# Optimization experiments

Measured on AMD Instinct MI355X. Metric: run time of the kernel, lower is better.

The kernel has to match this reference:

```python
import jax, jax.numpy as jnp
import numpy as np

H = 8
HD = 128
D = 1024
SCALE = 0.12
EOT = 50256
LN_EPS = 1e-6
THETA = 1024.0


def _layernorm(x, w):
    mu = jnp.mean(x, axis=-1, keepdims=True)
    var = jnp.mean(jnp.square(x - mu), axis=-1, keepdims=True)
    return (x - mu) * jax.lax.rsqrt(var + LN_EPS) * w


def _rmsnorm(x):
    eps = jnp.finfo(x.dtype).eps
    return x * jax.lax.rsqrt(jnp.mean(jnp.square(x), axis=-1, keepdims=True) + eps)


def _rope_tables(seq_len, head_dim):
    # half-truncated RoPE: only first half of the rotation pairs get nonzero freqs
    n = head_dim // 4
    freqs = (1.0 / THETA) ** jnp.linspace(0.0, 1.0, n)
    ang = jnp.concatenate([freqs, jnp.zeros((n,), freqs.dtype)])  # [head_dim//2]
    th = jnp.arange(seq_len, dtype=jnp.float32)[:, None] * ang[None, :]
    return jnp.cos(th), jnp.sin(th)  # each [S, head_dim//2]


def _apply_rope(x, cos, sin):
    # x: [B, S, H, hd]
    x1, x2 = jnp.split(x, 2, axis=-1)
    c = cos[None, :, None, :]
    s = sin[None, :, None, :]
    return jnp.concatenate([x1 * c + x2 * s, -x1 * s + x2 * c], axis=-1)


def setup_inputs() -> dict:
    key = jax.random.key(0)
    ks = jax.random.split(key, 10)
    B, S = 2, 2048
    return {
        "x": jax.random.normal(ks[0], (B, S, D), jnp.float32),
        "value_embed": jax.random.normal(ks[1], (S, D), jnp.float32),
        "x0": jax.random.normal(ks[2], (B, S, D), jnp.float32),
        "lambdas": jax.random.uniform(ks[3], (2,), jnp.float32),
        "sa_lambdas": jax.random.uniform(ks[4], (2,), jnp.float32),
        "ln1_w": jnp.ones((D,), jnp.float32),
        "ln2_w": jnp.ones((D,), jnp.float32),
        "w_qkv": jax.random.normal(ks[5], (D, 3 * D), jnp.float32) * 0.02,
        "w_o": jax.random.normal(ks[6], (D, D), jnp.float32) * 0.02,
        "w_fc": jax.random.normal(ks[7], (D, 4 * D), jnp.float32) * 0.02,
        "w_proj": jax.random.normal(ks[8], (4 * D, D), jnp.float32) * 0.02,
        "input_ids": jax.random.randint(ks[9], (S,), 0, 50257, jnp.int64),
    }


def reference(x, value_embed, x0, lambdas, sa_lambdas, ln1_w, ln2_w,
              w_qkv, w_o, w_fc, w_proj, input_ids):
    B, S, Dm = x.shape
    # U-Net residual mixing
    x = lambdas[0] * x + lambdas[1] * x0

    # attention branch
    xn = _layernorm(x, ln1_w)
    qkv = xn @ w_qkv                                # [B,S,3D]
    q, k, v = jnp.split(qkv, 3, axis=-1)
    q = q.reshape(B, S, H, HD)
    k = k.reshape(B, S, H, HD)
    v = v.reshape(B, S, H, HD)

    cos, sin = _rope_tables(S, HD)
    q = _apply_rope(q, cos, sin)
    k = _apply_rope(k, cos, sin)

    # value-embedding mixing
    ve = value_embed.reshape(S, H, HD)[None]        # [1,S,H,hd]
    v = sa_lambdas[0] * v + sa_lambdas[1] * ve

    # QK norm (unit-weight RMSNorm)
    q = _rmsnorm(q)
    k = _rmsnorm(k)

    # document-aware causal mask
    docs = jnp.cumsum(input_ids == EOT)
    idx = jnp.arange(S)
    mask = (idx[:, None] >= idx[None, :]) & (docs[:, None] == docs[None, :])

    scores = jnp.einsum("bqhd,bkhd->bhqk", q, k) * SCALE
    scores = jnp.where(mask[None, None], scores, -jnp.inf)
    attn = jax.nn.softmax(scores, axis=-1)
    out = jnp.einsum("bhqk,bkhd->bqhd", attn, v).reshape(B, S, Dm)
    x = x + out @ w_o

    # MLP with relu^2
    xn = _layernorm(x, ln2_w)
    h = jnp.square(jax.nn.relu(xn @ w_fc))
    x = x + h @ w_proj
    return x
```

## Files before the change

### kernel.cpp

```cpp
#include <hip/hip_runtime.h>

#define EOT_ID 50256

typedef __attribute__((ext_vector_type(8))) short bf16x8;
typedef __attribute__((ext_vector_type(4))) float f32x4;
typedef __attribute__((ext_vector_type(16))) float f32x16;

#define GLOAD_LDS(g, l)                                                        \
  __builtin_amdgcn_global_load_lds(                                            \
      (const __attribute__((address_space(1))) unsigned int*)(g),              \
      (__attribute__((address_space(3))) unsigned int*)(l), 16, 0, 0)

__device__ __forceinline__ unsigned short f2bf(float f) {
  union { float f; unsigned int u; } v; v.f = f;
  unsigned int r = v.u + 0x7FFFu + ((v.u >> 16) & 1u);
  return (unsigned short)(r >> 16);
}
__device__ __forceinline__ float bf2f(unsigned short b) {
  union { unsigned int u; float f; } v; v.u = ((unsigned int)b) << 16;
  return v.f;
}
__device__ __forceinline__ unsigned int cvtpk(float lo, float hi) {
  unsigned int r;
  asm("v_cvt_pk_bf16_f32 %0, %1, %2" : "=v"(r) : "v"(lo), "v"(hi));
  return r;
}
__device__ __forceinline__ void plswap(unsigned int& a, unsigned int& b) {
  asm volatile("v_permlane32_swap_b32 %0, %1" : "+v"(a), "+v"(b));
}
union U8 { unsigned int u[4]; bf16x8 v; };

__global__ void rope_tab_kernel(float* __restrict__ ct, float* __restrict__ st) {
  const int idx = blockIdx.x * 256 + threadIdx.x;
  const int s = idx >> 5, i = idx & 31;
  const float ang = (float)s * exp2f(-10.0f * (float)i / 31.0f);
  float sv, cv;
  sincosf(ang, &sv, &cv);
  ct[idx] = cv;
  st[idx] = sv;
}

__global__ __launch_bounds__(1024)
void docs_kernel(const int* __restrict__ ids, int* __restrict__ qstart) {
  __shared__ int a[2048], b2[2048];
  const int t = threadIdx.x;
  for (int i = t; i < 2048; i += 1024)
    a[i] = (ids[i] == EOT_ID) ? i : 0;
  __syncthreads();
  int* cur = a; int* nxt = b2;
  for (int off = 1; off < 2048; off <<= 1) {
    for (int i = t; i < 2048; i += 1024) {
      int v = cur[i];
      if (i >= off) { int u = cur[i - off]; v = (u > v) ? u : v; }
      nxt[i] = v;
    }
    __syncthreads();
    int* tmp = cur; cur = nxt; nxt = tmp;
  }
  for (int i = t; i < 2048; i += 1024) qstart[i] = cur[i];
}

__global__ __launch_bounds__(256)
void wtrans_kernel(const float* __restrict__ in, unsigned short* __restrict__ out,
                   int K, int N) {
  __shared__ float tile[32][33];
  const int nb = N >> 5;
  const int k0 = (blockIdx.x / nb) << 5, n0 = (blockIdx.x % nb) << 5;
  const int tx = threadIdx.x & 31, ty = threadIdx.x >> 5;
#pragma unroll
  for (int p = 0; p < 4; p++)
    tile[ty + p * 8][tx] = in[(size_t)(k0 + ty + p * 8) * N + n0 + tx];
  __syncthreads();
#pragma unroll
  for (int p = 0; p < 4; p++)
    out[(size_t)(n0 + ty + p * 8) * K + k0 + tx] = f2bf(tile[tx][ty + p * 8]);
}

template<bool MIX>
__global__ __launch_bounds__(256)
void ln_kernel(const float* __restrict__ x, const float* __restrict__ x0,
               const float* __restrict__ lam, const float* __restrict__ w,
               float* __restrict__ xm, unsigned short* __restrict__ xn) {
  __shared__ float red[8];
  const int row = blockIdx.x, t = threadIdx.x;
  const size_t base = (size_t)row << 10;
  float4 v = *(const float4*)(x + base + t * 4);
  if (MIX) {
    const float l0 = lam[0], l1 = lam[1];
    const float4 v0 = *(const float4*)(x0 + base + t * 4);
    v.x = l0 * v.x + l1 * v0.x;
    v.y = l0 * v.y + l1 * v0.y;
    v.z = l0 * v.z + l1 * v0.z;
    v.w = l0 * v.w + l1 * v0.w;
    *(float4*)(xm + base + t * 4) = v;
  }
  float s = v.x + v.y + v.z + v.w;
  float q = v.x * v.x + v.y * v.y + v.z * v.z + v.w * v.w;
#pragma unroll
  for (int off = 1; off < 64; off <<= 1) {
    s += __shfl_xor(s, off);
    q += __shfl_xor(q, off);
  }
  const int wid = t >> 6;
  if ((t & 63) == 0) { red[wid] = s; red[4 + wid] = q; }
  __syncthreads();
  s = red[0] + red[1] + red[2] + red[3];
  q = red[4] + red[5] + red[6] + red[7];
  const float mu = s * (1.0f / 1024.0f);
  const float var = q * (1.0f / 1024.0f) - mu * mu;
  const float rstd = rsqrtf(var + 1e-6f);
  const float4 wv = *(const float4*)(w + t * 4);
  ushort4 u;
  u.x = f2bf((v.x - mu) * rstd * wv.x);
  u.y = f2bf((v.y - mu) * rstd * wv.y);
  u.z = f2bf((v.z - mu) * rstd * wv.z);
  u.w = f2bf((v.w - mu) * rstd * wv.w);
  *(ushort4*)(xn + base + t * 4) = u;
}

template<int EPI, int BM, int BK>
__global__ __launch_bounds__(256, 4)
void gemm_bt(const unsigned short* __restrict__ A,
             const unsigned short* __restrict__ Bt,
             void* __restrict__ Cout,
             const float* __restrict__ res,
             int M, int N, int K) {
  __shared__ unsigned short As[2][BM * BK];
  __shared__ unsigned short Bs[2][128 * BK];
  const int t = threadIdx.x;
  const int wid = t >> 6;
  const int lane = t & 63;
  const int ln = lane & 15, kg = lane >> 4;
  const int nbm = M / BM;
  const int xcd = (int)blockIdx.x & 7, rr = (int)blockIdx.x >> 3;
  const int slab = nbm >> 3;
  const int bm = xcd * slab + (rr % slab);
  const int bn = rr / slab;
  const int m0 = bm * BM, n0 = bn << 7;
  const int wrow = (BM == 128) ? ((wid >> 1) * 64) : 0;
  const int wcol = (BM == 128) ? ((wid & 1) * 64) : (wid * 32);
  constexpr int NJ = (BM == 128) ? 4 : 2;
  constexpr int LA = BM * BK / 2048;
  constexpr int LB = 128 * BK / 2048;
  constexpr int KC = BK / 32;

  f32x4 acc[4][NJ] = {};

  const unsigned short* Abase = A + (size_t)m0 * K;
  const unsigned short* Bbase = Bt + (size_t)n0 * K;

  auto swz = [&](int row, int chunk) -> int {
    if constexpr (BK == 32) return chunk ^ ((row >> 1) & 3);
    else                    return chunk ^ (row & 7);
  };

  auto STAGE = [&](int bb, int kt) {
#pragma unroll
    for (int p = 0; p < LA; p++) {
      const int e = t * 8 + p * 2048;
      const int r = e / BK;
      const int cs = swz(r, (e >> 3) & (BK / 8 - 1));
      GLOAD_LDS(Abase + (size_t)r * K + kt + cs * 8, &As[bb][p * 2048 + wid * 512]);
    }
#pragma unroll
    for (int p = 0; p < LB; p++) {
      const int e = t * 8 + p * 2048;
      const int r = e / BK;
      const int cs = swz(r, (e >> 3) & (BK / 8 - 1));
      GLOAD_LDS(Bbase + (size_t)r * K + kt + cs * 8, &Bs[bb][p * 2048 + wid * 512]);
    }
  };

  STAGE(0, 0);
  int cur = 0;
  const int nk = K / BK;
  for (int ki = 0; ki < nk; ki++) {
    if (ki + 1 < nk) {
      STAGE(cur ^ 1, (ki + 1) * BK);
      if constexpr (LA + LB == 4)
        asm volatile("s_waitcnt vmcnt(4)" ::: "memory");
      else
        asm volatile("s_waitcnt vmcnt(6)" ::: "memory");
    } else {
      asm volatile("s_waitcnt vmcnt(0)" ::: "memory");
    }
    __builtin_amdgcn_s_barrier();

#pragma unroll
    for (int c = 0; c < KC; c++) {
      bf16x8 af[4], bfr[NJ];
#pragma unroll
      for (int i = 0; i < 4; i++) {
        const int ra = wrow + i * 16 + ln;
        af[i] = *(const bf16x8*)(&As[cur][ra * BK + swz(ra, c * 4 + kg) * 8]);
      }
#pragma unroll
      for (int j = 0; j < NJ; j++) {
        const int rb = wcol + j * 16 + ln;
        bfr[j] = *(const bf16x8*)(&Bs[cur][rb * BK + swz(rb, c * 4 + kg) * 8]);
      }
#pragma unroll
      for (int i = 0; i < 4; i++)
#pragma unroll
        for (int j = 0; j < NJ; j++)
          acc[i][j] = __builtin_amdgcn_mfma_f32_16x16x32_bf16(af[i], bfr[j], acc[i][j], 0, 0, 0);
    }

    __builtin_amdgcn_s_barrier();
    cur ^= 1;
  }

#pragma unroll
  for (int i = 0; i < 4; i++) {
#pragma unroll
    for (int j = 0; j < NJ; j++) {
#pragma unroll
      for (int r = 0; r < 4; r++) {
        const int row = m0 + wrow + i * 16 + kg * 4 + r;
        const int col = n0 + wcol + j * 16 + ln;
        const size_t idx = (size_t)row * N + col;
        float v = acc[i][j][r];
        if (EPI == 0) {
          ((float*)Cout)[idx] = v;
        } else if (EPI == 1) {
          ((float*)Cout)[idx] = v + res[idx];
        } else if (EPI == 2) {
          v = fmaxf(v, 0.0f);
          ((unsigned short*)Cout)[idx] = f2bf(v * v);
        } else {
          ((unsigned short*)Cout)[idx] = f2bf(v);
        }
      }
    }
  }
}

__global__ __launch_bounds__(256)
void rope_rms_kernel(const unsigned short* __restrict__ qkv,
                     const float* __restrict__ ct, const float* __restrict__ st,
                     const float* __restrict__ ve, const float* __restrict__ salam,
                     unsigned short* __restrict__ Qh, unsigned short* __restrict__ Kh,
                     unsigned short* __restrict__ Vt) {
  const int t = threadIdx.x;
  const int wid = t >> 6, i = t & 63;
  const int g = blockIdx.x * 4 + wid;
  const int b = g >> 14;
  const int s = (g >> 3) & 2047;
  const int h = g & 7;
  const unsigned short* base = qkv + (size_t)(b * 2048 + s) * 3072 + h * 128;
  float c = 1.0f, sn = 0.0f;
  if (i < 32) { c = ct[s * 32 + i]; sn = st[s * 32 + i]; }
  const float q1 = bf2f(base[i]), q2 = bf2f(base[64 + i]);
  const float k1 = bf2f(base[1024 + i]), k2 = bf2f(base[1024 + 64 + i]);
  const float q1r = q1 * c + q2 * sn, q2r = q2 * c - q1 * sn;
  const float k1r = k1 * c + k2 * sn, k2r = k2 * c - k1 * sn;
  float sq = q1r * q1r + q2r * q2r;
  float sk = k1r * k1r + k2r * k2r;
#pragma unroll
  for (int off = 1; off < 64; off <<= 1) {
    sq += __shfl_xor(sq, off);
    sk += __shfl_xor(sk, off);
  }
  const float eps = 1.1920929e-7f;
  const float rq = rsqrtf(sq * (1.0f / 128.0f) + eps);
  const float rk = rsqrtf(sk * (1.0f / 128.0f) + eps);
  unsigned short* qp = Qh + (((size_t)(b * 2048 + s) * 8 + h) << 7);
  unsigned short* kp = Kh + (((size_t)(b * 2048 + s) * 8 + h) << 7);
  qp[i] = f2bf(q1r * rq); qp[64 + i] = f2bf(q2r * rq);
  kp[i] = f2bf(k1r * rk); kp[64 + i] = f2bf(k2r * rk);
  const float l0 = salam[0], l1 = salam[1];
  const float* vep = ve + (size_t)s * 1024 + h * 128;
  const float v1 = l0 * bf2f(base[2048 + i]) + l1 * vep[i];
  const float v2 = l0 * bf2f(base[2048 + 64 + i]) + l1 * vep[64 + i];
  unsigned short* vp = Vt + (((size_t)(b * 8 + h) * 128) << 11) + s;
  vp[(size_t)i << 11] = f2bf(v1);
  vp[(size_t)(64 + i) << 11] = f2bf(v2);
}

__global__ __launch_bounds__(256, 2)
void attn_kernel(const unsigned short* __restrict__ Qh,
                 const unsigned short* __restrict__ Kh,
                 const unsigned short* __restrict__ Vt,
                 const int* __restrict__ qstart,
                 unsigned short* __restrict__ Out) {
  __shared__ char smem[65536];

  const int blk = blockIdx.x;
  const int p_ = blk >> 4;
  const int qt = (p_ < 16) ? (31 - p_) : (p_ - 16);
  const int bh = blk & 15;
  const int b = bh >> 3, h = bh & 7;
  const int q0 = qt << 6;
  const int t = threadIdx.x;
  const int wid = t >> 6, lane = t & 63;
  const int qw = wid & 1, kw = wid >> 1;
  const int ln5 = lane & 31, hi = lane >> 5;
  const int qrow = q0 + qw * 32;
  const int tp = qw * 64 + lane;

  bf16x8 qf[8];
  {
    const unsigned short* qp =
        Qh + (((size_t)(b * 2048 + qrow + ln5) * 8 + h) << 7) + hi * 8;
#pragma unroll
    for (int c = 0; c < 8; c++) qf[c] = *(const bf16x8*)(qp + c * 16);
  }
  const int qid = qrow + ln5;
  const int qs = qstart[qid];
  int qsmax = qs;
#pragma unroll
  for (int off = 1; off < 32; off <<= 1)
    qsmax = max(qsmax, __shfl_xor(qsmax, off));

  float m = -64.0f, l = 0.0f;
  f32x16 o[4] = {};

  const int kt0 = qstart[q0] & ~31;
  const int T = (q0 + 64 - kt0) >> 5;
  const float SC = 0.12f * 1.4426950408889634f;

  unsigned short* Kb = (unsigned short*)(smem + kw * 16384);
  unsigned short* Vb = (unsigned short*)(smem + 32768 + kw * 16384);

  auto STAGE = [&](int bb, int kt) {
#pragma unroll
    for (int r = 0; r < 4; r++) {
      const int e = tp * 16 + r * 2048;
      const int row = e >> 8;
      const int ch = (e >> 4) & 15;
      const int sch = ch ^ ((row ^ (row >> 3)) & 7);
      GLOAD_LDS(Kh + (((size_t)(b * 2048 + kt + row) * 8 + h) << 7) + sch * 8,
                (char*)Kb + bb * 8192 + r * 2048 + qw * 1024 + (lane << 4));
    }
#pragma unroll
    for (int r = 0; r < 4; r++) {
      const int e = tp * 16 + r * 2048;
      const int row = e >> 6;
      const int ch = (e >> 4) & 3;
      const int sch = ch ^ ((row >> 1) & 3);
      GLOAD_LDS(Vt + (((size_t)((b * 8 + h) * 128 + row)) << 11) + kt + sch * 8,
                (char*)Vb + bb * 8192 + r * 2048 + qw * 1024 + (lane << 4));
    }
  };

  STAGE(0, kt0 + kw * 32);
  int cur = 0;
  const int nLoop = (T + 1) >> 1;

  for (int i = 0; i < nLoop; i++) {
    const int tid = 2 * i + kw;
    const bool hasnext = (tid + 2) < T;
    if (hasnext) {
      STAGE(cur ^ 1, kt0 + (tid + 2) * 32);
      asm volatile("s_waitcnt vmcnt(8)" ::: "memory");
    } else {
      asm volatile("s_waitcnt vmcnt(0)" ::: "memory");
    }
    __builtin_amdgcn_s_barrier();

    if (tid < T) {
      const int kt = kt0 + tid * 32;
      const unsigned short* ksb = (const unsigned short*)((char*)Kb + cur * 8192);
      const unsigned short* vsb = (const unsigned short*)((char*)Vb + cur * 8192);

      f32x16 sacc = {};
      {
        const int key = ln5;
        const int kx = (key ^ (key >> 3)) & 7;
        const unsigned short* krow = &ksb[key * 128];
#pragma unroll
        for (int c = 0; c < 8; c++) {
          bf16x8 kf = *(const bf16x8*)(krow + (((2 * c + hi) ^ kx) << 3));
          sacc = __builtin_amdgcn_mfma_f32_32x32x16_bf16(kf, qf[c], sacc, 0, 0, 0);
        }
      }

      const bool full = (kt + 32 <= qrow) && (kt >= qsmax);

      float p[16];
      float mx = -1e30f;
      if (full) {
#pragma unroll
        for (int i2 = 0; i2 < 16; i2++) {
          const float ts = sacc[i2] * SC;
          p[i2] = ts;
          mx = fmaxf(mx, ts);
        }
      } else {
#pragma unroll
        for (int i2 = 0; i2 < 16; i2++) {
          const int key = kt + (i2 & 3) + 8 * (i2 >> 2) + 4 * hi;
          const bool valid = (key <= qid) && (key >= qs);
          const float ts = valid ? sacc[i2] * SC : -1e30f;
          p[i2] = ts;
          mx = fmaxf(mx, ts);
        }
      }
      mx = fmaxf(mx, __shfl_xor(mx, 32));

      const bool dresc = __any(mx - m > 8.0f);
      if (dresc) {
        const float mn = fmaxf(m, mx);
        const float fac = exp2f(m - mn);
        m = mn;
        l *= fac;
#pragma unroll
        for (int r = 0; r < 16; r++) {
          const float fr = __shfl(fac, (r & 3) + 8 * (r >> 2) + 4 * hi);
          o[0][r] *= fr; o[1][r] *= fr; o[2][r] *= fr; o[3][r] *= fr;
        }
      }

      float sum = 0.0f;
#pragma unroll
      for (int i2 = 0; i2 < 16; i2++) {
        const float pv = exp2f(p[i2] - m);
        p[i2] = pv;
        sum += pv;
      }
      sum += __shfl_xor(sum, 32);
      l += sum;

      bf16x8 pa[2];
#pragma unroll
      for (int bb2 = 0; bb2 < 2; bb2++) {
        unsigned int a0 = cvtpk(p[bb2 * 8 + 0], p[bb2 * 8 + 1]);
        unsigned int b0 = cvtpk(p[bb2 * 8 + 4], p[bb2 * 8 + 5]);
        unsigned int a1 = cvtpk(p[bb2 * 8 + 2], p[bb2 * 8 + 3]);
        unsigned int b1 = cvtpk(p[bb2 * 8 + 6], p[bb2 * 8 + 7]);
        plswap(a0, b0);
        plswap(a1, b1);
        U8 u; u.u[0] = a0; u.u[1] = a1; u.u[2] = b0; u.u[3] = b1;
        pa[bb2] = u.v;
      }

#pragma unroll
      for (int dt = 0; dt < 4; dt++) {
        const int d = dt * 32 + ln5;
        const int dx = (d >> 1) & 3;
        const unsigned short* vrow = &vsb[d * 32];
#pragma unroll
        for (int ks = 0; ks < 2; ks++) {
          bf16x8 vf = *(const bf16x8*)(vrow + (((2 * ks + hi) ^ dx) << 3));
          o[dt] = __builtin_amdgcn_mfma_f32_32x32x16_bf16(pa[ks], vf, o[dt], 0, 0, 0);
        }
      }
    }

    __builtin_amdgcn_s_barrier();
    cur ^= 1;
  }

  __syncthreads();
  float* oex = (float*)smem;
  float* mlx = (float*)(smem + 32768);
  if (kw == 1) {
    if (lane < 32) {
      mlx[(qw * 32 + lane) * 2 + 0] = m;
      mlx[(qw * 32 + lane) * 2 + 1] = l;
    }
    float* dst = oex + (qw * 64 + lane) * 64;
#pragma unroll
    for (int dt = 0; dt < 4; dt++)
#pragma unroll
      for (int r = 0; r < 16; r++) dst[dt * 16 + r] = o[dt][r];
  }
  __syncthreads();
  if (kw == 0) {
    const float m1 = mlx[(qw * 32 + ln5) * 2 + 0];
    const float l1 = mlx[(qw * 32 + ln5) * 2 + 1];
    const float ms = fmaxf(m, m1);
    const float a0 = exp2f(m - ms), a1 = exp2f(m1 - ms);
    const float inv = 1.0f / (l * a0 + l1 * a1);
    const float* src = oex + (qw * 64 + lane) * 64;
#pragma unroll
    for (int r = 0; r < 16; r++) {
      const int crow = (r & 3) + 8 * (r >> 2) + 4 * hi;
      const float a0r = __shfl(a0, crow);
      const float a1r = __shfl(a1, crow);
      const float ivr = __shfl(inv, crow);
      const int q = qrow + crow;
      unsigned short* op = Out + (((size_t)(b * 2048 + q)) << 10) + h * 128 + ln5;
#pragma unroll
      for (int dt = 0; dt < 4; dt++)
        op[dt * 32] = f2bf((o[dt][r] * a0r + src[dt * 16 + r] * a1r) * ivr);
    }
  }
}

extern "C" void kernel_launch(void* const* d_in, const int* in_sizes, int n_in,
                              void* d_out, int out_size, void* d_ws, size_t ws_size,
                              hipStream_t stream) {
  const float* x     = (const float*)d_in[0];
  const float* vemb  = (const float*)d_in[1];
  const float* x0    = (const float*)d_in[2];
  const float* lam   = (const float*)d_in[3];
  const float* slam  = (const float*)d_in[4];
  const float* ln1w  = (const float*)d_in[5];
  const float* ln2w  = (const float*)d_in[6];
  const float* wqkv  = (const float*)d_in[7];
  const float* wo    = (const float*)d_in[8];
  const float* wfc   = (const float*)d_in[9];
  const float* wproj = (const float*)d_in[10];
  const int*   ids   = (const int*)d_in[11];

  char* ws = (char*)d_ws;
  unsigned short* wqkvT  = (unsigned short*)(ws + 0);
  unsigned short* woT    = (unsigned short*)(ws + 6291456);
  unsigned short* wfcT   = (unsigned short*)(ws + 8388608);
  unsigned short* wprojT = (unsigned short*)(ws + 16777216);
  float*          xm     = (float*)(ws + 25165824);
  unsigned short* qkv    = (unsigned short*)(ws + 41943040);
  unsigned short* hbuf   = (unsigned short*)(ws + 41943040);
  unsigned short* xn1    = (unsigned short*)(ws + 92274688);
  unsigned short* ao     = (unsigned short*)(ws + 92274688);
  unsigned short* qh     = (unsigned short*)(ws + 100663296);
  unsigned short* xn2    = (unsigned short*)(ws + 100663296);
  unsigned short* kh     = (unsigned short*)(ws + 109051904);
  unsigned short* vt     = (unsigned short*)(ws + 117440512);
  float*          x2     = (float*)(ws + 109051904);
  float*          ctab   = (float*)(ws + 125829120);
  float*          stab   = (float*)(ws + 126091264);
  int*            qstart = (int*)(ws + 126353408);

  rope_tab_kernel<<<dim3(256), dim3(256), 0, stream>>>(ctab, stab);
  docs_kernel<<<dim3(1), dim3(1024), 0, stream>>>(ids, qstart);
  wtrans_kernel<<<dim3(32 * 96), dim3(256), 0, stream>>>(wqkv, wqkvT, 1024, 3072);
  wtrans_kernel<<<dim3(32 * 32), dim3(256), 0, stream>>>(wo, woT, 1024, 1024);
  wtrans_kernel<<<dim3(32 * 128), dim3(256), 0, stream>>>(wfc, wfcT, 1024, 4096);
  wtrans_kernel<<<dim3(128 * 32), dim3(256), 0, stream>>>(wproj, wprojT, 4096, 1024);

  ln_kernel<true><<<dim3(4096), dim3(256), 0, stream>>>(x, x0, lam, ln1w, xm, xn1);
  gemm_bt<3, 128, 32><<<dim3(32 * 24), dim3(256), 0, stream>>>(xn1, wqkvT, (void*)qkv,
                                                               (const float*)nullptr, 4096, 3072, 1024);
  rope_rms_kernel<<<dim3(8192), dim3(256), 0, stream>>>(qkv, ctab, stab, vemb, slam, qh, kh, vt);
  attn_kernel<<<dim3(512), dim3(256), 0, stream>>>(qh, kh, vt, qstart, ao);
  gemm_bt<1, 64, 64><<<dim3(64 * 8), dim3(256), 0, stream>>>(ao, woT, (void*)x2, xm, 4096, 1024, 1024);
  ln_kernel<false><<<dim3(4096), dim3(256), 0, stream>>>(x2, (const float*)nullptr,
                                                         (const float*)nullptr, ln2w,
                                                         (float*)nullptr, xn2);
  gemm_bt<2, 128, 32><<<dim3(32 * 32), dim3(256), 0, stream>>>(xn2, wfcT, (void*)hbuf,
                                                               (const float*)nullptr, 4096, 4096, 1024);
  gemm_bt<1, 64, 64><<<dim3(64 * 8), dim3(256), 0, stream>>>(hbuf, wprojT, d_out, x2, 4096, 1024, 4096);
}
```

Before: 268.2 us.

## Split-K the MLP down-projection GEMM into two halves with a reduction kernel

```diff
diff --git a/kernel.cpp b/kernel.cpp
--- a/kernel.cpp
+++ b/kernel.cpp
@@ -74,6 +74,16 @@
 #pragma unroll
   for (int p = 0; p < 4; p++)
     out[(size_t)(n0 + ty + p * 8) * K + k0 + tx] = f2bf(tile[tx][ty + p * 8]);
+}
+
+__global__ __launch_bounds__(256)
+void add2_kernel(const float* __restrict__ a, const float* __restrict__ b,
+                 float* __restrict__ out) {
+  const int i = (blockIdx.x * 256 + threadIdx.x) * 4;
+  float4 va = *(const float4*)(a + i);
+  const float4 vb = *(const float4*)(b + i);
+  va.x += vb.x; va.y += vb.y; va.z += vb.z; va.w += vb.w;
+  *(float4*)(out + i) = va;
 }
 
 template<bool MIX>
@@ -118,21 +128,29 @@
   *(ushort4*)(xn + base + t * 4) = u;
 }
 
-template<int EPI, int BM, int BK>
+template<int EPI, int BM, int BK, bool KSPLIT>
 __global__ __launch_bounds__(256, 4)
 void gemm_bt(const unsigned short* __restrict__ A,
              const unsigned short* __restrict__ Bt,
              void* __restrict__ Cout,
              const float* __restrict__ res,
-             int M, int N, int K) {
+             int M, int N, int K,
+             float* __restrict__ Cout2) {
   __shared__ unsigned short As[2][BM * BK];
   __shared__ unsigned short Bs[2][128 * BK];
   const int t = threadIdx.x;
   const int wid = t >> 6;
   const int lane = t & 63;
   const int ln = lane & 15, kg = lane >> 4;
+  int blkid = (int)blockIdx.x;
+  int half = 0;
+  if constexpr (KSPLIT) {
+    const int hg = (int)gridDim.x >> 1;
+    half = (blkid >= hg) ? 1 : 0;
+    blkid -= half * hg;
+  }
   const int nbm = M / BM;
-  const int xcd = (int)blockIdx.x & 7, rr = (int)blockIdx.x >> 3;
+  const int xcd = blkid & 7, rr = blkid >> 3;
   const int slab = nbm >> 3;
   const int bm = xcd * slab + (rr % slab);
   const int bn = rr / slab;
@@ -144,6 +162,9 @@
   constexpr int LB = 128 * BK / 2048;
   constexpr int KC = BK / 32;
 
+  const int koff = KSPLIT ? half * (K >> 1) : 0;
+  const int klen = KSPLIT ? (K >> 1) : K;
+
   f32x4 acc[4][NJ] = {};
 
   const unsigned short* Abase = A + (size_t)m0 * K;
@@ -171,13 +192,15 @@
     }
   };
 
-  STAGE(0, 0);
+  STAGE(0, koff);
   int cur = 0;
-  const int nk = K / BK;
+  const int nk = klen / BK;
   for (int ki = 0; ki < nk; ki++) {
     if (ki + 1 < nk) {
-      STAGE(cur ^ 1, (ki + 1) * BK);
-      if constexpr (LA + LB == 4)
+      STAGE(cur ^ 1, koff + (ki + 1) * BK);
+      if constexpr (LA + LB == 3)
+        asm volatile("s_waitcnt vmcnt(3)" ::: "memory");
+      else if constexpr (LA + LB == 4)
         asm volatile("s_waitcnt vmcnt(4)" ::: "memory");
       else
         asm volatile("s_waitcnt vmcnt(6)" ::: "memory");
@@ -220,7 +243,10 @@
         const int col = n0 + wcol + j * 16 + ln;
         const size_t idx = (size_t)row * N + col;
         float v = acc[i][j][r];
-        if (EPI == 0) {
+        if constexpr (KSPLIT) {
+          if (half == 0) ((float*)Cout)[idx] = v + res[idx];
+          else           Cout2[idx] = v;
+        } else if (EPI == 0) {
           ((float*)Cout)[idx] = v;
         } else if (EPI == 1) {
           ((float*)Cout)[idx] = v + res[idx];
@@ -510,10 +536,12 @@
   unsigned short* wfcT   = (unsigned short*)(ws + 8388608);
   unsigned short* wprojT = (unsigned short*)(ws + 16777216);
   float*          xm     = (float*)(ws + 25165824);
+  float*          P0     = (float*)(ws + 25165824);
   unsigned short* qkv    = (unsigned short*)(ws + 41943040);
   unsigned short* hbuf   = (unsigned short*)(ws + 41943040);
   unsigned short* xn1    = (unsigned short*)(ws + 92274688);
   unsigned short* ao     = (unsigned short*)(ws + 92274688);
+  float*          P1     = (float*)(ws + 92274688);
   unsigned short* qh     = (unsigned short*)(ws + 100663296);
   unsigned short* xn2    = (unsigned short*)(ws + 100663296);
   unsigned short* kh     = (unsigned short*)(ws + 109051904);
@@ -531,15 +559,18 @@
   wtrans_kernel<<<dim3(128 * 32), dim3(256), 0, stream>>>(wproj, wprojT, 4096, 1024);
 
   ln_kernel<true><<<dim3(4096), dim3(256), 0, stream>>>(x, x0, lam, ln1w, xm, xn1);
-  gemm_bt<3, 128, 32><<<dim3(32 * 24), dim3(256), 0, stream>>>(xn1, wqkvT, (void*)qkv,
-                                                               (const float*)nullptr, 4096, 3072, 1024);
+  gemm_bt<3, 128, 32, false><<<dim3(32 * 24), dim3(256), 0, stream>>>(
+      xn1, wqkvT, (void*)qkv, (const float*)nullptr, 4096, 3072, 1024, nullptr);
   rope_rms_kernel<<<dim3(8192), dim3(256), 0, stream>>>(qkv, ctab, stab, vemb, slam, qh, kh, vt);
   attn_kernel<<<dim3(512), dim3(256), 0, stream>>>(qh, kh, vt, qstart, ao);
-  gemm_bt<1, 64, 64><<<dim3(64 * 8), dim3(256), 0, stream>>>(ao, woT, (void*)x2, xm, 4096, 1024, 1024);
+  gemm_bt<1, 64, 64, false><<<dim3(64 * 8), dim3(256), 0, stream>>>(
+      ao, woT, (void*)x2, xm, 4096, 1024, 1024, nullptr);
   ln_kernel<false><<<dim3(4096), dim3(256), 0, stream>>>(x2, (const float*)nullptr,
                                                          (const float*)nullptr, ln2w,
                                                          (float*)nullptr, xn2);
-  gemm_bt<2, 128, 32><<<dim3(32 * 32), dim3(256), 0, stream>>>(xn2, wfcT, (void*)hbuf,
-                                                               (const float*)nullptr, 4096, 4096, 1024);
-  gemm_bt<1, 64, 64><<<dim3(64 * 8), dim3(256), 0, stream>>>(hbuf, wprojT, d_out, x2, 4096, 1024, 4096);
-}
+  gemm_bt<2, 128, 32, false><<<dim3(32 * 32), dim3(256), 0, stream>>>(
+      xn2, wfcT, (void*)hbuf, (const float*)nullptr, 4096, 4096, 1024, nullptr);
+  gemm_bt<1, 64, 32, true><<<dim3(128 * 8), dim3(256), 0, stream>>>(
+      hbuf, wprojT, (void*)P0, x2, 4096, 1024, 4096, P1);
+  add2_kernel<<<dim3(4096), dim3(256), 0, stream>>>(P0, P1, (float*)d_out);
+}
```

New measurement: 282.6 us. 1.05x slower.

## Add 256x256-tile 8-wave GEMM with phased LDS pipeline for QKV and FC

Applied to the files above, without the earlier changes.

```diff
diff --git a/kernel.cpp b/kernel.cpp
--- a/kernel.cpp
+++ b/kernel.cpp
@@ -235,6 +235,148 @@
   }
 }
 
+#define SWZ9(x) ((x) ^ ((((x) >> 9) & 1) << 5))
+
+#define RD_A(BUF, QM)                                                          \
+  {                                                                            \
+    const char* sb_ = smem + (((BUF)*2 + 0) * 2 + (QM)) * 16384;               \
+    _Pragma("unroll") for (int i_ = 0; i_ < 4; i_++)                           \
+    _Pragma("unroll") for (int kc_ = 0; kc_ < 2; kc_++) {                      \
+      int x_ = kc_ * 8192 + (wr * 64 + i_ * 16 + ln) * 64 + kg * 16;           \
+      Af[i_][kc_] = *(const bf16x8*)(sb_ + SWZ9(x_));                          \
+    }                                                                          \
+  }
+
+#define RD_B(BUF, QN, BARR)                                                    \
+  {                                                                            \
+    const char* sb_ = smem + (((BUF)*2 + 1) * 2 + (QN)) * 16384;               \
+    _Pragma("unroll") for (int j_ = 0; j_ < 2; j_++)                           \
+    _Pragma("unroll") for (int kc_ = 0; kc_ < 2; kc_++) {                      \
+      int x_ = kc_ * 8192 + (wc * 32 + j_ * 16 + ln) * 64 + kg * 16;           \
+      BARR[j_][kc_] = *(const bf16x8*)(sb_ + SWZ9(x_));                        \
+    }                                                                          \
+  }
+
+#define MFMAQ(QM, QN, BARR)                                                    \
+  _Pragma("unroll") for (int i_ = 0; i_ < 4; i_++)                             \
+  _Pragma("unroll") for (int j_ = 0; j_ < 2; j_++)                             \
+  _Pragma("unroll") for (int kc_ = 0; kc_ < 2; kc_++)                          \
+    acc[QM][QN][i_][j_] = __builtin_amdgcn_mfma_f32_16x16x32_bf16(             \
+        Af[i_][kc_], BARR[j_][kc_], acc[QM][QN][i_][j_], 0, 0, 0);
+
+#define PHTAIL()                                                               \
+  __builtin_amdgcn_s_barrier();                                                \
+  asm volatile("s_waitcnt lgkmcnt(0)" ::: "memory");                           \
+  __builtin_amdgcn_sched_barrier(0);                                           \
+  __builtin_amdgcn_s_setprio(1)
+
+#define PHEND()                                                                \
+  __builtin_amdgcn_s_setprio(0);                                               \
+  __builtin_amdgcn_s_barrier()
+
+template<int EPI>
+__global__ __launch_bounds__(512, 2)
+void gemm256(const unsigned short* __restrict__ A,
+             const unsigned short* __restrict__ Bt,
+             void* __restrict__ Cout,
+             int M, int N, int K) {
+  extern __shared__ char smem[];
+  const int tid = threadIdx.x;
+  const int wid = tid >> 6, lane = tid & 63;
+  const int wr = wid >> 2, wc = wid & 3;
+  const int ln = lane & 15, kg = lane >> 4;
+  const int nbm = M >> 8;
+  const int xcd = (int)blockIdx.x & 7, rr = (int)blockIdx.x >> 3;
+  const int slab = nbm >> 3;
+  const int bm = xcd * slab + (rr % slab);
+  const int bn = rr / slab;
+  const int m0 = bm << 8, n0 = bn << 8;
+  const size_t K2 = (size_t)K * 2;
+  const char* Ac = (const char*)A;
+  const char* Bc = (const char*)Bt;
+
+  f32x4 acc[2][2][4][2] = {};
+  bf16x8 Af[4][2], B0[2][2], B1[2][2];
+
+  auto STG = [&](int buf, int ab, int h, int tile) {
+    const char* gb = ab ? Bc : Ac;
+    const int ro = (ab ? n0 : m0) + h * 128;
+    char* db = smem + ((buf * 2 + ab) * 2 + h) * 16384;
+#pragma unroll
+    for (int q = 0; q < 2; q++) {
+      const int p0 = q * 8192 + tid * 16;
+      const int lin = SWZ9(p0);
+      GLOAD_LDS(gb + (size_t)(ro + ((lin >> 6) & 127)) * K2 +
+                    (size_t)tile * 128 + (lin >> 13) * 64 + (lin & 63),
+                db + p0);
+    }
+  };
+
+  STG(0, 0, 0, 0); STG(0, 0, 1, 0); STG(0, 1, 0, 0); STG(0, 1, 1, 0);
+  STG(1, 0, 0, 1); STG(1, 1, 0, 1); STG(1, 1, 1, 1);
+  asm volatile("s_waitcnt vmcnt(6)" ::: "memory");
+  __builtin_amdgcn_s_barrier();
+
+  const int niter = K >> 7;
+  for (int it = 0; it < niter; it++) {
+    const int tA = 2 * it, tB = tA + 1;
+    const bool more = (it + 1 < niter);
+
+    RD_A(0, 0); RD_B(0, 0, B0);
+    STG(1, 0, 1, tB);
+    PHTAIL(); MFMAQ(0, 0, B0); PHEND();
+    RD_B(0, 1, B1);
+    if (more) STG(0, 0, 0, tA + 2);
+    PHTAIL(); MFMAQ(0, 1, B1); PHEND();
+    RD_A(0, 1);
+    if (more) STG(0, 1, 0, tA + 2);
+    PHTAIL(); MFMAQ(1, 0, B0); PHEND();
+    if (more) {
+      STG(0, 1, 1, tA + 2);
+      asm volatile("s_waitcnt vmcnt(6)" ::: "memory");
+    } else {
+      asm volatile("s_waitcnt vmcnt(0)" ::: "memory");
+    }
+    PHTAIL(); MFMAQ(1, 1, B1); PHEND();
+    RD_A(1, 0); RD_B(1, 0, B0);
+    if (more) STG(0, 0, 1, tA + 2);
+    PHTAIL(); MFMAQ(0, 0, B0); PHEND();
+    RD_B(1, 1, B1);
+    if (more) STG(1, 0, 0, tB + 2);
+    PHTAIL(); MFMAQ(0, 1, B1); PHEND();
+    RD_A(1, 1);
+    if (more) STG(1, 1, 0, tB + 2);
+    PHTAIL(); MFMAQ(1, 0, B0); PHEND();
+    if (more) {
+      STG(1, 1, 1, tB + 2);
+      asm volatile("s_waitcnt vmcnt(6)" ::: "memory");
+    }
+    PHTAIL(); MFMAQ(1, 1, B1); PHEND();
+  }
+
+#pragma unroll
+  for (int qm = 0; qm < 2; qm++)
+#pragma unroll
+    for (int qn = 0; qn < 2; qn++)
+#pragma unroll
+      for (int i = 0; i < 4; i++)
+#pragma unroll
+        for (int j = 0; j < 2; j++)
+#pragma unroll
+          for (int r = 0; r < 4; r++) {
+            const int row = m0 + qm * 128 + wr * 64 + i * 16 + kg * 4 + r;
+            const int col = n0 + qn * 128 + wc * 32 + j * 16 + ln;
+            const size_t idx = (size_t)row * N + col;
+            float v = acc[qm][qn][i][j][r];
+            if (EPI == 2) {
+              v = fmaxf(v, 0.0f);
+              ((unsigned short*)Cout)[idx] = f2bf(v * v);
+            } else {
+              ((unsigned short*)Cout)[idx] = f2bf(v);
+            }
+          }
+}
+
 __global__ __launch_bounds__(256)
 void rope_rms_kernel(const unsigned short* __restrict__ qkv,
                      const float* __restrict__ ct, const float* __restrict__ st,
@@ -283,7 +425,7 @@
                  const unsigned short* __restrict__ Vt,
                  const int* __restrict__ qstart,
                  unsigned short* __restrict__ Out) {
-  __shared__ char smem[65536];
+  __shared__ char asmem[65536];
 
   const int blk = blockIdx.x;
   const int p_ = blk >> 4;
@@ -319,8 +461,8 @@
   const int T = (q0 + 64 - kt0) >> 5;
   const float SC = 0.12f * 1.4426950408889634f;
 
-  unsigned short* Kb = (unsigned short*)(smem + kw * 16384);
-  unsigned short* Vb = (unsigned short*)(smem + 32768 + kw * 16384);
+  unsigned short* Kb = (unsigned short*)(asmem + kw * 16384);
+  unsigned short* Vb = (unsigned short*)(asmem + 32768 + kw * 16384);
 
   auto STAGE = [&](int bb, int kt) {
 #pragma unroll
@@ -348,18 +490,18 @@
   const int nLoop = (T + 1) >> 1;
 
   for (int i = 0; i < nLoop; i++) {
-    const int tid = 2 * i + kw;
-    const bool hasnext = (tid + 2) < T;
+    const int tid2 = 2 * i + kw;
+    const bool hasnext = (tid2 + 2) < T;
     if (hasnext) {
-      STAGE(cur ^ 1, kt0 + (tid + 2) * 32);
+      STAGE(cur ^ 1, kt0 + (tid2 + 2) * 32);
       asm volatile("s_waitcnt vmcnt(8)" ::: "memory");
     } else {
       asm volatile("s_waitcnt vmcnt(0)" ::: "memory");
     }
     __builtin_amdgcn_s_barrier();
 
-    if (tid < T) {
-      const int kt = kt0 + tid * 32;
+    if (tid2 < T) {
+      const int kt = kt0 + tid2 * 32;
       const unsigned short* ksb = (const unsigned short*)((char*)Kb + cur * 8192);
       const unsigned short* vsb = (const unsigned short*)((char*)Vb + cur * 8192);
 
@@ -452,8 +594,8 @@
   }
 
   __syncthreads();
-  float* oex = (float*)smem;
-  float* mlx = (float*)(smem + 32768);
+  float* oex = (float*)asmem;
+  float* mlx = (float*)(asmem + 32768);
   if (kw == 1) {
     if (lane < 32) {
       mlx[(qw * 32 + lane) * 2 + 0] = m;
@@ -523,6 +665,15 @@
   float*          stab   = (float*)(ws + 126091264);
   int*            qstart = (int*)(ws + 126353408);
 
+  static int attr_done = 0;
+  if (!attr_done) {
+    hipFuncSetAttribute((const void*)gemm256<3>,
+                        hipFuncAttributeMaxDynamicSharedMemorySize, 131072);
+    hipFuncSetAttribute((const void*)gemm256<2>,
+                        hipFuncAttributeMaxDynamicSharedMemorySize, 131072);
+    attr_done = 1;
+  }
+
   rope_tab_kernel<<<dim3(256), dim3(256), 0, stream>>>(ctab, stab);
   docs_kernel<<<dim3(1), dim3(1024), 0, stream>>>(ids, qstart);
   wtrans_kernel<<<dim3(32 * 96), dim3(256), 0, stream>>>(wqkv, wqkvT, 1024, 3072);
@@ -531,15 +682,17 @@
   wtrans_kernel<<<dim3(128 * 32), dim3(256), 0, stream>>>(wproj, wprojT, 4096, 1024);
 
   ln_kernel<true><<<dim3(4096), dim3(256), 0, stream>>>(x, x0, lam, ln1w, xm, xn1);
-  gemm_bt<3, 128, 32><<<dim3(32 * 24), dim3(256), 0, stream>>>(xn1, wqkvT, (void*)qkv,
-                                                               (const float*)nullptr, 4096, 3072, 1024);
+  gemm256<3><<<dim3(192), dim3(512), 131072, stream>>>(xn1, wqkvT, (void*)qkv,
+                                                       4096, 3072, 1024);
   rope_rms_kernel<<<dim3(8192), dim3(256), 0, stream>>>(qkv, ctab, stab, vemb, slam, qh, kh, vt);
   attn_kernel<<<dim3(512), dim3(256), 0, stream>>>(qh, kh, vt, qstart, ao);
-  gemm_bt<1, 64, 64><<<dim3(64 * 8), dim3(256), 0, stream>>>(ao, woT, (void*)x2, xm, 4096, 1024, 1024);
+  gemm_bt<1, 64, 64><<<dim3(64 * 8), dim3(256), 0, stream>>>(ao, woT, (void*)x2, xm,
+                                                             4096, 1024, 1024);
   ln_kernel<false><<<dim3(4096), dim3(256), 0, stream>>>(x2, (const float*)nullptr,
                                                          (const float*)nullptr, ln2w,
                                                          (float*)nullptr, xn2);
-  gemm_bt<2, 128, 32><<<dim3(32 * 32), dim3(256), 0, stream>>>(xn2, wfcT, (void*)hbuf,
-                                                               (const float*)nullptr, 4096, 4096, 1024);
-  gemm_bt<1, 64, 64><<<dim3(64 * 8), dim3(256), 0, stream>>>(hbuf, wprojT, d_out, x2, 4096, 1024, 4096);
-}
+  gemm256<2><<<dim3(256), dim3(512), 131072, stream>>>(xn2, wfcT, (void*)hbuf,
+                                                       4096, 4096, 1024);
+  gemm_bt<1, 64, 64><<<dim3(64 * 8), dim3(256), 0, stream>>>(hbuf, wprojT, d_out, x2,
+                                                             4096, 1024, 4096);
+}
```

After: 261.9 us. -2.4%, faster.
